# Performance work log

Measured on AMD Instinct MI355X. Metric: run time of the kernel, lower is better.

Reference implementation:

```python
import jax, jax.numpy as jnp
import numpy as np

N = 16384            # number of input vectors
CODEBOOK_SIZE = 8192  # M
DIM = 256             # dim_feature
BETA = 0.25           # commitment_weight


def setup_inputs() -> dict:
    key = jax.random.key(0)
    kx, ke = jax.random.split(key)
    x = jax.random.normal(kx, (N, DIM), dtype=jnp.float32)
    # kaiming-uniform-style init for the codebook
    bound = float(np.sqrt(3.0 / DIM))
    embeddings = jax.random.uniform(ke, (CODEBOOK_SIZE, DIM), dtype=jnp.float32,
                                    minval=-bound, maxval=bound)
    return {"x": x, "embeddings": embeddings}


def reference(x, embeddings):
    # l2_dist: sqrt(sum((x_i - e_j)^2)) computed via the GEMM expansion
    x2 = jnp.sum(x * x, axis=1, keepdims=True)               # (N, 1)
    e2 = jnp.sum(embeddings * embeddings, axis=1)            # (M,)
    d2 = x2 + e2[None, :] - 2.0 * (x @ embeddings.T)         # (N, M)
    dist = jnp.sqrt(jnp.maximum(d2, 0.0))
    # deterministic gumbel_sample path (training eval / stochastic=False):
    # argmax of logits = -dist  <=>  argmin of dist
    ind = jnp.argmin(dist, axis=1)                           # (N,)
    quantized = embeddings[ind]                              # one_hot @ embeddings
    # commitment loss: beta * ||x_q - sg(x)||^2 (docstring)
    commit_loss = BETA * jnp.mean((quantized - jax.lax.stop_gradient(x)) ** 2)
    # straight-through estimator
    quantized_st = x + jax.lax.stop_gradient(quantized - x)
    # perplexity from per-code counts (one-hot scatter)
    counts = jnp.zeros((CODEBOOK_SIZE,), jnp.float32).at[ind].add(1.0)
    probs = counts / counts.sum()
    perplexity = jnp.exp(-jnp.sum(probs * jnp.log(probs + 1e-10)))
    return quantized_st, ind, commit_loss, perplexity
```

## Files before the change

### kernel.cpp

```cpp
#include <hip/hip_runtime.h>
#include <stdint.h>


#define N_VEC 16384
#define M_CODES 8192
#define DIM 256
#define BETA 0.25f

#define NSLICE 8
#define SLICE_CODES 1024
#define BM 128
#define BN 128
#define BK 32
#define NPART 16

typedef __attribute__((ext_vector_type(4))) float f32x4;
typedef __attribute__((ext_vector_type(8))) __bf16 bf16x8;

__device__ __forceinline__ void gll16(const void* g, const void* lds) {
    __builtin_amdgcn_global_load_lds(
        (const __attribute__((address_space(1))) uint32_t*)(uintptr_t)g,
        (__attribute__((address_space(3))) uint32_t*)(uint32_t)(uintptr_t)lds,
        16, 0, 0);
}

__device__ __forceinline__ ushort f2bf(float f) {
    uint32_t u = __float_as_uint(f);
    return (ushort)((u + 0x7FFFu + ((u >> 16) & 1u)) >> 16);
}
__device__ __forceinline__ float bf2f(ushort h) {
    return __uint_as_float(((uint32_t)h) << 16);
}

__global__ __launch_bounds__(256) void split_kernel(const float* __restrict__ in,
                                                    ushort* __restrict__ hi,
                                                    ushort* __restrict__ lo) {
    int i = (blockIdx.x * 256 + threadIdx.x) * 4;
    float4 v = *(const float4*)(in + i);
    ushort h0 = f2bf(v.x), h1 = f2bf(v.y), h2 = f2bf(v.z), h3 = f2bf(v.w);
    ushort l0 = f2bf(v.x - bf2f(h0)), l1 = f2bf(v.y - bf2f(h1));
    ushort l2 = f2bf(v.z - bf2f(h2)), l3 = f2bf(v.w - bf2f(h3));
    *(ushort4*)(hi + i) = make_ushort4(h0, h1, h2, h3);
    *(ushort4*)(lo + i) = make_ushort4(l0, l1, l2, l3);
}

__global__ __launch_bounds__(256) void e2_kernel(const float* __restrict__ emb,
                                                 float* __restrict__ e2) {
    int wave = threadIdx.x >> 6;
    int lane = threadIdx.x & 63;
    int code = blockIdx.x * 4 + wave;
    float4 v = *(const float4*)(emb + code * DIM + lane * 4);
    float s = v.x * v.x + v.y * v.y + v.z * v.z + v.w * v.w;
    #pragma unroll
    for (int off = 32; off; off >>= 1) s += __shfl_xor(s, off);
    if (lane == 0) e2[code] = s;
}

__global__ __launch_bounds__(256) void vq_mfma_kernel(
    const ushort* __restrict__ xh, const ushort* __restrict__ xl,
    const ushort* __restrict__ eh, const ushort* __restrict__ el,
    const float* __restrict__ e2g, unsigned long long* __restrict__ partials) {
    __shared__ char lds[4 * BM * BK * 2];

    const int t = threadIdx.x;
    const int lane = t & 63;
    const int wv = t >> 6;
    const int lane15 = lane & 15;
    const int l16 = lane >> 4;

    const int bid = blockIdx.x;
    const int rt = bid & 127;
    const int slice = bid >> 7;
    const int row0 = rt * BM;
    const int cslice0 = slice * SLICE_CODES;

    const int wr0 = (wv & 1) * 64;
    const int wc0 = (wv >> 1) * 64;

    int byteA[4], byteB[4];
    #pragma unroll
    for (int f = 0; f < 4; ++f) {
        int ra = wr0 + f * 16 + lane15;
        byteA[f] = ra * 64 + (((l16 ^ (ra >> 1)) & 3) << 4);
        int rb = wc0 + f * 16 + lane15;
        byteB[f] = rb * 64 + (((l16 ^ (rb >> 1)) & 3) << 4);
    }

    const int s0 = wv * 128 + lane;
    const int s1 = s0 + 64;
    const int r0s = s0 >> 2, r1s = s1 >> 2;
    const int c0s = ((s0 & 3) ^ ((s0 >> 3) & 3)) << 3;
    const int c1s = ((s1 & 3) ^ ((s1 >> 3) & 3)) << 3;
    const size_t xoff0 = (size_t)(row0 + r0s) * DIM + c0s;
    const size_t xoff1 = (size_t)(row0 + r1s) * DIM + c1s;
    const size_t eoff0 = (size_t)(cslice0 + r0s) * DIM + c0s;
    const size_t eoff1 = (size_t)(cslice0 + r1s) * DIM + c1s;
    char* ldq0 = lds + wv * 2048;
    char* ldq1 = lds + wv * 2048 + 1024;

    float best[16];
    int bidx[16];
    #pragma unroll
    for (int s = 0; s < 16; ++s) { best[s] = __uint_as_float(0x7f800000u); bidx[s] = 0; }

    for (int ct = 0; ct < SLICE_CODES / BN; ++ct) {
        f32x4 acc[4][4];
        #pragma unroll
        for (int fi = 0; fi < 4; ++fi)
            #pragma unroll
            for (int fj = 0; fj < 4; ++fj) acc[fi][fj] = (f32x4){0.f, 0.f, 0.f, 0.f};

        const ushort* ehp0 = eh + eoff0 + (size_t)ct * BN * DIM;
        const ushort* ehp1 = eh + eoff1 + (size_t)ct * BN * DIM;
        const ushort* elp0 = el + eoff0 + (size_t)ct * BN * DIM;
        const ushort* elp1 = el + eoff1 + (size_t)ct * BN * DIM;

        for (int kc = 0; kc < DIM / BK; ++kc) {
            const int ko = kc * BK;
            gll16(xh + xoff0 + ko, ldq0);
            gll16(xh + xoff1 + ko, ldq1);
            gll16(xl + xoff0 + ko, ldq0 + 8192);
            gll16(xl + xoff1 + ko, ldq1 + 8192);
            gll16(ehp0 + ko, ldq0 + 16384);
            gll16(ehp1 + ko, ldq1 + 16384);
            gll16(elp0 + ko, ldq0 + 24576);
            gll16(elp1 + ko, ldq1 + 24576);
            __syncthreads();

            bf16x8 ah[4], alo[4], bh[4], blo[4];
            #pragma unroll
            for (int f = 0; f < 4; ++f) {
                ah[f]  = *(const bf16x8*)(lds + byteA[f]);
                alo[f] = *(const bf16x8*)(lds + 8192 + byteA[f]);
                bh[f]  = *(const bf16x8*)(lds + 16384 + byteB[f]);
                blo[f] = *(const bf16x8*)(lds + 24576 + byteB[f]);
            }
            #pragma unroll
            for (int fi = 0; fi < 4; ++fi)
                #pragma unroll
                for (int fj = 0; fj < 4; ++fj) {
                    acc[fi][fj] = __builtin_amdgcn_mfma_f32_16x16x32_bf16(
                        ah[fi], bh[fj], acc[fi][fj], 0, 0, 0);
                    acc[fi][fj] = __builtin_amdgcn_mfma_f32_16x16x32_bf16(
                        ah[fi], blo[fj], acc[fi][fj], 0, 0, 0);
                    acc[fi][fj] = __builtin_amdgcn_mfma_f32_16x16x32_bf16(
                        alo[fi], bh[fj], acc[fi][fj], 0, 0, 0);
                }
            __syncthreads();
        }

        const int cb = cslice0 + ct * BN + wc0;
        #pragma unroll
        for (int fj = 0; fj < 4; ++fj) {
            const int c = cb + fj * 16 + lane15;
            const float e2v = e2g[c];
            #pragma unroll
            for (int fi = 0; fi < 4; ++fi)
                #pragma unroll
                for (int r = 0; r < 4; ++r) {
                    float sc = e2v - 2.0f * acc[fi][fj][r];
                    const int slot = fi * 4 + r;
                    if (sc < best[slot]) { best[slot] = sc; bidx[slot] = c; }
                }
        }
    }

    #pragma unroll
    for (int slot = 0; slot < 16; ++slot) {
        float v = best[slot];
        int ix = bidx[slot];
        #pragma unroll
        for (int off = 1; off < 16; off <<= 1) {
            float v2 = __shfl_xor(v, off);
            int ix2 = __shfl_xor(ix, off);
            if (v2 < v || (v2 == v && ix2 < ix)) { v = v2; ix = ix2; }
        }
        if (lane15 == 0) {
            int fi = slot >> 2, r = slot & 3;
            int row = row0 + wr0 + fi * 16 + l16 * 4 + r;
            uint32_t u = __float_as_uint(v);
            uint32_t ord = (u & 0x80000000u) ? ~u : (u | 0x80000000u);
            partials[(size_t)(slice * 2 + (wv >> 1)) * N_VEC + row] =
                ((unsigned long long)ord << 32) | (unsigned)ix;
        }
    }
}

__global__ __launch_bounds__(256) void reduce_kernel(
    const unsigned long long* __restrict__ partials, float* __restrict__ out_ind,
    int* __restrict__ ws_ind, unsigned* __restrict__ counts) {
    int row = blockIdx.x * 256 + threadIdx.x;
    unsigned long long m = partials[row];
    #pragma unroll
    for (int s = 1; s < NPART; ++s) {
        unsigned long long v = partials[(size_t)s * N_VEC + row];
        if (v < m) m = v;
    }
    int ix = (int)(unsigned)(m & 0xFFFFFFFFull);
    out_ind[row] = (float)ix;
    ws_ind[row] = ix;
    atomicAdd(&counts[ix], 1u);
}

__global__ __launch_bounds__(256) void gather_kernel(
    const float* __restrict__ x, const float* __restrict__ emb,
    const int* __restrict__ ws_ind, float* __restrict__ out_q,
    float* __restrict__ loss_acc) {
    __shared__ float partial[4];
    int wave = threadIdx.x >> 6;
    int lane = threadIdx.x & 63;
    int row = blockIdx.x * 4 + wave;
    int idx = ws_ind[row];
    float4 q = *(const float4*)(emb + idx * DIM + lane * 4);
    float4 xv = *(const float4*)(x + row * DIM + lane * 4);
    *(float4*)(out_q + row * DIM + lane * 4) = q;
    float dx = q.x - xv.x, dy = q.y - xv.y, dz = q.z - xv.z, dw = q.w - xv.w;
    float s = dx * dx + dy * dy + dz * dz + dw * dw;
    #pragma unroll
    for (int off = 32; off; off >>= 1) s += __shfl_xor(s, off);
    if (lane == 0) partial[wave] = s;
    __syncthreads();
    if (threadIdx.x == 0)
        atomicAdd(loss_acc, partial[0] + partial[1] + partial[2] + partial[3]);
}

__global__ __launch_bounds__(256) void finalize_kernel(
    const unsigned* __restrict__ counts, const float* __restrict__ loss_acc,
    float* __restrict__ out_scalars) {
    __shared__ float red[256];
    float h = 0.0f;
    for (int c = threadIdx.x; c < M_CODES; c += 256) {
        float p = (float)counts[c] * (1.0f / (float)N_VEC);
        h += p * logf(p + 1e-10f);
    }
    red[threadIdx.x] = h;
    __syncthreads();
    for (int s = 128; s; s >>= 1) {
        if (threadIdx.x < s) red[threadIdx.x] += red[threadIdx.x + s];
        __syncthreads();
    }
    if (threadIdx.x == 0) {
        out_scalars[0] = BETA * loss_acc[0] / (float)(N_VEC * DIM);
        out_scalars[1] = expf(-red[0]);
    }
}

extern "C" void kernel_launch(void* const* d_in, const int* in_sizes, int n_in,
                              void* d_out, int out_size, void* d_ws, size_t ws_size,
                              hipStream_t stream) {
    const float* x = (const float*)d_in[0];
    const float* emb = (const float*)d_in[1];

    float* out = (float*)d_out;
    float* out_q = out;
    float* out_ind = out + (size_t)N_VEC * DIM;
    float* out_scalars = out_ind + N_VEC;

    ushort* xh = (ushort*)out;
    ushort* xl = xh + (size_t)N_VEC * DIM;

    char* wp = (char*)d_ws;
    ushort* eh = (ushort*)wp;  wp += (size_t)M_CODES * DIM * 2;
    ushort* el = (ushort*)wp;  wp += (size_t)M_CODES * DIM * 2;
    float* e2 = (float*)wp;    wp += (size_t)M_CODES * 4;
    unsigned long long* partials = (unsigned long long*)wp;
    wp += (size_t)NPART * N_VEC * 8;
    unsigned* counts = (unsigned*)wp; wp += (size_t)M_CODES * 4;
    int* ws_ind = (int*)wp;    wp += (size_t)N_VEC * 4;
    float* loss_acc = (float*)wp;

    hipMemsetAsync(counts, 0, M_CODES * 4, stream);
    hipMemsetAsync(loss_acc, 0, 4, stream);

    split_kernel<<<N_VEC * DIM / 1024, 256, 0, stream>>>(x, xh, xl);
    split_kernel<<<M_CODES * DIM / 1024, 256, 0, stream>>>(emb, eh, el);
    e2_kernel<<<M_CODES / 4, 256, 0, stream>>>(emb, e2);

    vq_mfma_kernel<<<128 * NSLICE, 256, 0, stream>>>(xh, xl, eh, el, e2, partials);

    reduce_kernel<<<N_VEC / 256, 256, 0, stream>>>(partials, out_ind, ws_ind, counts);
    gather_kernel<<<N_VEC / 4, 256, 0, stream>>>(x, emb, ws_ind, out_q, loss_acc);
    finalize_kernel<<<1, 256, 0, stream>>>(counts, loss_acc, out_scalars);
}
```

Before: 297.9 us.

## Double-buffer MFMA kernel LDS loads and fuse prep and finish kernels

The MFMA distance kernel now uses two 32KB LDS buffers and issues global-to-LDS loads for the next k-step while computing the current one. The code-tile and k loops are flattened into one loop, with launch bounds asking for two blocks per CU. The three prep kernels (split x, split emb, e2) are fused into one, and the reduce and gather kernels are merged into a finish kernel that does a wave-shuffle argmin. This cuts launch count and exposed load latency, at the cost of double LDS (64KB per block), which may limit occupancy.

```diff
diff --git a/kernel.cpp b/kernel.cpp
--- a/kernel.cpp
+++ b/kernel.cpp
@@ -13,6 +13,7 @@
 #define BN 128
 #define BK 32
 #define NPART 16
+#define LDS_HALF 32768
 
 typedef __attribute__((ext_vector_type(4))) float f32x4;
 typedef __attribute__((ext_vector_type(8))) __bf16 bf16x8;
@@ -24,6 +25,11 @@
         16, 0, 0);
 }
 
+#define PIPE_SYNC() do { \
+    asm volatile("s_waitcnt vmcnt(0)" ::: "memory"); \
+    asm volatile("s_barrier" ::: "memory"); \
+} while (0)
+
 __device__ __forceinline__ ushort f2bf(float f) {
     uint32_t u = __float_as_uint(f);
     return (ushort)((u + 0x7FFFu + ((u >> 16) & 1u)) >> 16);
@@ -32,35 +38,50 @@
     return __uint_as_float(((uint32_t)h) << 16);
 }
 
-__global__ __launch_bounds__(256) void split_kernel(const float* __restrict__ in,
-                                                    ushort* __restrict__ hi,
-                                                    ushort* __restrict__ lo) {
-    int i = (blockIdx.x * 256 + threadIdx.x) * 4;
-    float4 v = *(const float4*)(in + i);
+__global__ __launch_bounds__(256) void prep_kernel(
+    const float* __restrict__ x, const float* __restrict__ emb,
+    ushort* __restrict__ xh, ushort* __restrict__ xl,
+    ushort* __restrict__ eh, ushort* __restrict__ el,
+    float* __restrict__ e2) {
+    const int wave = threadIdx.x >> 6;
+    const int lane = threadIdx.x & 63;
+    const int row = blockIdx.x * 4 + wave;
+
+    const float* src;
+    ushort* ph;
+    ushort* pl;
+    bool is_e;
+    int er = row - N_VEC;
+    if (row < N_VEC) {
+        src = x + (size_t)row * DIM;
+        ph = xh + (size_t)row * DIM;
+        pl = xl + (size_t)row * DIM;
+        is_e = false;
+    } else {
+        src = emb + (size_t)er * DIM;
+        ph = eh + (size_t)er * DIM;
+        pl = el + (size_t)er * DIM;
+        is_e = true;
+    }
+    float4 v = *(const float4*)(src + lane * 4);
     ushort h0 = f2bf(v.x), h1 = f2bf(v.y), h2 = f2bf(v.z), h3 = f2bf(v.w);
     ushort l0 = f2bf(v.x - bf2f(h0)), l1 = f2bf(v.y - bf2f(h1));
     ushort l2 = f2bf(v.z - bf2f(h2)), l3 = f2bf(v.w - bf2f(h3));
-    *(ushort4*)(hi + i) = make_ushort4(h0, h1, h2, h3);
-    *(ushort4*)(lo + i) = make_ushort4(l0, l1, l2, l3);
-}
-
-__global__ __launch_bounds__(256) void e2_kernel(const float* __restrict__ emb,
-                                                 float* __restrict__ e2) {
-    int wave = threadIdx.x >> 6;
-    int lane = threadIdx.x & 63;
-    int code = blockIdx.x * 4 + wave;
-    float4 v = *(const float4*)(emb + code * DIM + lane * 4);
-    float s = v.x * v.x + v.y * v.y + v.z * v.z + v.w * v.w;
-    #pragma unroll
-    for (int off = 32; off; off >>= 1) s += __shfl_xor(s, off);
-    if (lane == 0) e2[code] = s;
-}
-
-__global__ __launch_bounds__(256) void vq_mfma_kernel(
+    *(ushort4*)(ph + lane * 4) = make_ushort4(h0, h1, h2, h3);
+    *(ushort4*)(pl + lane * 4) = make_ushort4(l0, l1, l2, l3);
+    if (is_e) {
+        float s = v.x * v.x + v.y * v.y + v.z * v.z + v.w * v.w;
+        #pragma unroll
+        for (int off = 32; off; off >>= 1) s += __shfl_xor(s, off);
+        if (lane == 0) e2[er] = s;
+    }
+}
+
+__global__ __launch_bounds__(256, 2) void vq_mfma_kernel(
     const ushort* __restrict__ xh, const ushort* __restrict__ xl,
     const ushort* __restrict__ eh, const ushort* __restrict__ el,
     const float* __restrict__ e2g, unsigned long long* __restrict__ partials) {
-    __shared__ char lds[4 * BM * BK * 2];
+    extern __shared__ char lds[];
 
     const int t = threadIdx.x;
     const int lane = t & 63;
@@ -91,77 +112,104 @@
     const int r0s = s0 >> 2, r1s = s1 >> 2;
     const int c0s = ((s0 & 3) ^ ((s0 >> 3) & 3)) << 3;
     const int c1s = ((s1 & 3) ^ ((s1 >> 3) & 3)) << 3;
-    const size_t xoff0 = (size_t)(row0 + r0s) * DIM + c0s;
-    const size_t xoff1 = (size_t)(row0 + r1s) * DIM + c1s;
-    const size_t eoff0 = (size_t)(cslice0 + r0s) * DIM + c0s;
-    const size_t eoff1 = (size_t)(cslice0 + r1s) * DIM + c1s;
-    char* ldq0 = lds + wv * 2048;
-    char* ldq1 = lds + wv * 2048 + 1024;
+    const ushort* pxh0 = xh + (size_t)(row0 + r0s) * DIM + c0s;
+    const ushort* pxh1 = xh + (size_t)(row0 + r1s) * DIM + c1s;
+    const ushort* pxl0 = xl + (size_t)(row0 + r0s) * DIM + c0s;
+    const ushort* pxl1 = xl + (size_t)(row0 + r1s) * DIM + c1s;
+    const ushort* peh0 = eh + (size_t)(cslice0 + r0s) * DIM + c0s;
+    const ushort* peh1 = eh + (size_t)(cslice0 + r1s) * DIM + c1s;
+    const ushort* pel0 = el + (size_t)(cslice0 + r0s) * DIM + c0s;
+    const ushort* pel1 = el + (size_t)(cslice0 + r1s) * DIM + c1s;
 
     float best[16];
     int bidx[16];
     #pragma unroll
     for (int s = 0; s < 16; ++s) { best[s] = __uint_as_float(0x7f800000u); bidx[s] = 0; }
 
-    for (int ct = 0; ct < SLICE_CODES / BN; ++ct) {
-        f32x4 acc[4][4];
+    f32x4 acc[4][4];
+    #pragma unroll
+    for (int fi = 0; fi < 4; ++fi)
+        #pragma unroll
+        for (int fj = 0; fj < 4; ++fj) acc[fi][fj] = (f32x4){0.f, 0.f, 0.f, 0.f};
+
+    auto stage = [&](int buf, int ks) {
+        const int ct = ks >> 3;
+        const int kc = ks & 7;
+        const size_t xo = (size_t)(kc << 5);
+        const size_t eo = (size_t)ct * ((size_t)BN * DIM) + (kc << 5);
+        char* l0 = lds + buf * LDS_HALF + wv * 2048;
+        char* l1 = l0 + 1024;
+        gll16(pxh0 + xo, l0);
+        gll16(pxh1 + xo, l1);
+        gll16(pxl0 + xo, l0 + 8192);
+        gll16(pxl1 + xo, l1 + 8192);
+        gll16(peh0 + eo, l0 + 16384);
+        gll16(peh1 + eo, l1 + 16384);
+        gll16(pel0 + eo, l0 + 24576);
+        gll16(pel1 + eo, l1 + 24576);
+    };
+
+    stage(0, 0);
+    PIPE_SYNC();
+
+    int cur = 0;
+    for (int ks = 0; ks < 64; ++ks) {
+        if (ks < 63) stage(cur ^ 1, ks + 1);
+
+        const char* lb = lds + cur * LDS_HALF;
+        bf16x8 ah[4], bh[4];
+        #pragma unroll
+        for (int f = 0; f < 4; ++f) {
+            ah[f] = *(const bf16x8*)(lb + byteA[f]);
+            bh[f] = *(const bf16x8*)(lb + 16384 + byteB[f]);
+        }
         #pragma unroll
         for (int fi = 0; fi < 4; ++fi)
             #pragma unroll
-            for (int fj = 0; fj < 4; ++fj) acc[fi][fj] = (f32x4){0.f, 0.f, 0.f, 0.f};
-
-        const ushort* ehp0 = eh + eoff0 + (size_t)ct * BN * DIM;
-        const ushort* ehp1 = eh + eoff1 + (size_t)ct * BN * DIM;
-        const ushort* elp0 = el + eoff0 + (size_t)ct * BN * DIM;
-        const ushort* elp1 = el + eoff1 + (size_t)ct * BN * DIM;
-
-        for (int kc = 0; kc < DIM / BK; ++kc) {
-            const int ko = kc * BK;
-            gll16(xh + xoff0 + ko, ldq0);
-            gll16(xh + xoff1 + ko, ldq1);
-            gll16(xl + xoff0 + ko, ldq0 + 8192);
-            gll16(xl + xoff1 + ko, ldq1 + 8192);
-            gll16(ehp0 + ko, ldq0 + 16384);
-            gll16(ehp1 + ko, ldq1 + 16384);
-            gll16(elp0 + ko, ldq0 + 24576);
-            gll16(elp1 + ko, ldq1 + 24576);
-            __syncthreads();
-
-            bf16x8 ah[4], alo[4], bh[4], blo[4];
-            #pragma unroll
-            for (int f = 0; f < 4; ++f) {
-                ah[f]  = *(const bf16x8*)(lds + byteA[f]);
-                alo[f] = *(const bf16x8*)(lds + 8192 + byteA[f]);
-                bh[f]  = *(const bf16x8*)(lds + 16384 + byteB[f]);
-                blo[f] = *(const bf16x8*)(lds + 24576 + byteB[f]);
+            for (int fj = 0; fj < 4; ++fj)
+                acc[fi][fj] = __builtin_amdgcn_mfma_f32_16x16x32_bf16(
+                    ah[fi], bh[fj], acc[fi][fj], 0, 0, 0);
+        bf16x8 blo[4];
+        #pragma unroll
+        for (int f = 0; f < 4; ++f) blo[f] = *(const bf16x8*)(lb + 24576 + byteB[f]);
+        #pragma unroll
+        for (int fi = 0; fi < 4; ++fi)
+            #pragma unroll
+            for (int fj = 0; fj < 4; ++fj)
+                acc[fi][fj] = __builtin_amdgcn_mfma_f32_16x16x32_bf16(
+                    ah[fi], blo[fj], acc[fi][fj], 0, 0, 0);
+        bf16x8 alo[4];
+        #pragma unroll
+        for (int f = 0; f < 4; ++f) alo[f] = *(const bf16x8*)(lb + 8192 + byteA[f]);
+        #pragma unroll
+        for (int fi = 0; fi < 4; ++fi)
+            #pragma unroll
+            for (int fj = 0; fj < 4; ++fj)
+                acc[fi][fj] = __builtin_amdgcn_mfma_f32_16x16x32_bf16(
+                    alo[fi], bh[fj], acc[fi][fj], 0, 0, 0);
+
+        PIPE_SYNC();
+        cur ^= 1;
+
+        if ((ks & 7) == 7) {
+            const int cb = cslice0 + (ks >> 3) * BN + wc0;
+            #pragma unroll
+            for (int fj = 0; fj < 4; ++fj) {
+                const int c = cb + fj * 16 + lane15;
+                const float e2v = e2g[c];
+                #pragma unroll
+                for (int fi = 0; fi < 4; ++fi)
+                    #pragma unroll
+                    for (int r = 0; r < 4; ++r) {
+                        float sc = e2v - 2.0f * acc[fi][fj][r];
+                        const int slot = fi * 4 + r;
+                        if (sc < best[slot]) { best[slot] = sc; bidx[slot] = c; }
+                    }
             }
             #pragma unroll
             for (int fi = 0; fi < 4; ++fi)
                 #pragma unroll
-                for (int fj = 0; fj < 4; ++fj) {
-                    acc[fi][fj] = __builtin_amdgcn_mfma_f32_16x16x32_bf16(
-                        ah[fi], bh[fj], acc[fi][fj], 0, 0, 0);
-                    acc[fi][fj] = __builtin_amdgcn_mfma_f32_16x16x32_bf16(
-                        ah[fi], blo[fj], acc[fi][fj], 0, 0, 0);
-                    acc[fi][fj] = __builtin_amdgcn_mfma_f32_16x16x32_bf16(
-                        alo[fi], bh[fj], acc[fi][fj], 0, 0, 0);
-                }
-            __syncthreads();
-        }
-
-        const int cb = cslice0 + ct * BN + wc0;
-        #pragma unroll
-        for (int fj = 0; fj < 4; ++fj) {
-            const int c = cb + fj * 16 + lane15;
-            const float e2v = e2g[c];
-            #pragma unroll
-            for (int fi = 0; fi < 4; ++fi)
-                #pragma unroll
-                for (int r = 0; r < 4; ++r) {
-                    float sc = e2v - 2.0f * acc[fi][fj][r];
-                    const int slot = fi * 4 + r;
-                    if (sc < best[slot]) { best[slot] = sc; bidx[slot] = c; }
-                }
+                for (int fj = 0; fj < 4; ++fj) acc[fi][fj] = (f32x4){0.f, 0.f, 0.f, 0.f};
         }
     }
 
@@ -186,39 +234,38 @@
     }
 }
 
-__global__ __launch_bounds__(256) void reduce_kernel(
-    const unsigned long long* __restrict__ partials, float* __restrict__ out_ind,
-    int* __restrict__ ws_ind, unsigned* __restrict__ counts) {
-    int row = blockIdx.x * 256 + threadIdx.x;
-    unsigned long long m = partials[row];
-    #pragma unroll
-    for (int s = 1; s < NPART; ++s) {
-        unsigned long long v = partials[(size_t)s * N_VEC + row];
+__global__ __launch_bounds__(256) void finish_kernel(
+    const float* __restrict__ x, const float* __restrict__ emb,
+    const unsigned long long* __restrict__ partials,
+    float* __restrict__ out_ind, float* __restrict__ out_q,
+    unsigned* __restrict__ counts, float* __restrict__ loss_acc) {
+    __shared__ float partial[4];
+    const int wave = threadIdx.x >> 6;
+    const int lane = threadIdx.x & 63;
+    const int row = blockIdx.x * 4 + wave;
+
+    unsigned long long m = ~0ull;
+    if (lane < NPART) m = partials[(size_t)lane * N_VEC + row];
+    #pragma unroll
+    for (int off = 1; off < NPART; off <<= 1) {
+        unsigned long long v = __shfl_xor(m, off);
         if (v < m) m = v;
     }
-    int ix = (int)(unsigned)(m & 0xFFFFFFFFull);
-    out_ind[row] = (float)ix;
-    ws_ind[row] = ix;
-    atomicAdd(&counts[ix], 1u);
-}
-
-__global__ __launch_bounds__(256) void gather_kernel(
-    const float* __restrict__ x, const float* __restrict__ emb,
-    const int* __restrict__ ws_ind, float* __restrict__ out_q,
-    float* __restrict__ loss_acc) {
-    __shared__ float partial[4];
-    int wave = threadIdx.x >> 6;
-    int lane = threadIdx.x & 63;
-    int row = blockIdx.x * 4 + wave;
-    int idx = ws_ind[row];
-    float4 q = *(const float4*)(emb + idx * DIM + lane * 4);
-    float4 xv = *(const float4*)(x + row * DIM + lane * 4);
-    *(float4*)(out_q + row * DIM + lane * 4) = q;
+    m = __shfl(m, 0);
+    const int ix = (int)(unsigned)(m & 0xFFFFFFFFull);
+
+    float4 q = *(const float4*)(emb + (size_t)ix * DIM + lane * 4);
+    float4 xv = *(const float4*)(x + (size_t)row * DIM + lane * 4);
+    *(float4*)(out_q + (size_t)row * DIM + lane * 4) = q;
     float dx = q.x - xv.x, dy = q.y - xv.y, dz = q.z - xv.z, dw = q.w - xv.w;
     float s = dx * dx + dy * dy + dz * dz + dw * dw;
     #pragma unroll
     for (int off = 32; off; off >>= 1) s += __shfl_xor(s, off);
-    if (lane == 0) partial[wave] = s;
+    if (lane == 0) {
+        out_ind[row] = (float)ix;
+        atomicAdd(&counts[ix], 1u);
+        partial[wave] = s;
+    }
     __syncthreads();
     if (threadIdx.x == 0)
         atomicAdd(loss_acc, partial[0] + partial[1] + partial[2] + partial[3]);
@@ -266,19 +313,19 @@
     unsigned long long* partials = (unsigned long long*)wp;
     wp += (size_t)NPART * N_VEC * 8;
     unsigned* counts = (unsigned*)wp; wp += (size_t)M_CODES * 4;
-    int* ws_ind = (int*)wp;    wp += (size_t)N_VEC * 4;
     float* loss_acc = (float*)wp;
 
     hipMemsetAsync(counts, 0, M_CODES * 4, stream);
     hipMemsetAsync(loss_acc, 0, 4, stream);
 
-    split_kernel<<<N_VEC * DIM / 1024, 256, 0, stream>>>(x, xh, xl);
-    split_kernel<<<M_CODES * DIM / 1024, 256, 0, stream>>>(emb, eh, el);
-    e2_kernel<<<M_CODES / 4, 256, 0, stream>>>(emb, e2);
-
-    vq_mfma_kernel<<<128 * NSLICE, 256, 0, stream>>>(xh, xl, eh, el, e2, partials);
-
-    reduce_kernel<<<N_VEC / 256, 256, 0, stream>>>(partials, out_ind, ws_ind, counts);
-    gather_kernel<<<N_VEC / 4, 256, 0, stream>>>(x, emb, ws_ind, out_q, loss_acc);
+    prep_kernel<<<(N_VEC + M_CODES) / 4, 256, 0, stream>>>(x, emb, xh, xl, eh, el, e2);
+
+    hipFuncSetAttribute((const void*)vq_mfma_kernel,
+                        hipFuncAttributeMaxDynamicSharedMemorySize, 2 * LDS_HALF);
+    vq_mfma_kernel<<<128 * NSLICE, 256, 2 * LDS_HALF, stream>>>(xh, xl, eh, el, e2,
+                                                                partials);
+
+    finish_kernel<<<N_VEC / 4, 256, 0, stream>>>(x, emb, partials, out_ind, out_q,
+                                                 counts, loss_acc);
     finalize_kernel<<<1, 256, 0, stream>>>(counts, loss_acc, out_scalars);
 }
```

After: 277.2 us. -7.0%, faster.
